# Performance work log

Measured on AMD Instinct MI355X. Metric: run time of the kernel, lower is better.

The kernel has to match this reference:

```python
import jax, jax.numpy as jnp
import numpy as np

GRID = 14  # encoded_image_size

def _grid_edge_index():
    # Exact replica of build_adjacency_matrix().nonzero(): 8-neighbor 14x14 grid.
    edges = []
    for r in range(GRID):
        for c in range(GRID):
            i = r * GRID + c
            for rr in range(max(0, r - 1), min(r + 2, GRID)):
                for cc in range(max(0, c - 1), min(c + 2, GRID)):
                    if rr == r and cc == c:
                        continue
                    edges.append((i, rr * GRID + cc))
    return np.asarray(edges, dtype=np.int64).T  # (2, 1404)


def setup_inputs() -> dict:
    key = jax.random.key(0)
    k1, k2, k3 = jax.random.split(key, 3)
    B, H, W, C, Hid = 128, 14, 14, 2048, 1024
    x = jax.random.normal(k1, (B, H, W, C), dtype=jnp.float32)
    edge_index = jnp.asarray(_grid_edge_index())
    W1 = jax.random.normal(k2, (C, Hid), dtype=jnp.float32) * (1.0 / np.sqrt(C))
    b1 = jnp.zeros((Hid,), jnp.float32)
    W2 = jax.random.normal(k3, (Hid, C), dtype=jnp.float32) * (1.0 / np.sqrt(Hid))
    b2 = jnp.zeros((C,), jnp.float32)
    return {"x": x, "edge_index": edge_index, "W1": W1, "b1": b1, "W2": W2, "b2": b2}


def _gcn_conv(h, W, b, src, dst, dinv):
    # PyG GCNConv: linear transform, symmetric deg-normalized (A+I) aggregation, bias.
    h = h @ W  # [N, out]
    norm = (dinv[src] * dinv[dst])[:, None]
    agg = jax.ops.segment_sum(h[src] * norm, dst, num_segments=h.shape[0])
    agg = agg + h * (dinv * dinv)[:, None]  # self-loop term, norm = 1/deg_i
    return agg + b


def reference(x, edge_index, W1, b1, W2, b2):
    B, H, Wd, C = x.shape
    N = B * H * Wd
    # Faithful to original: permute(0,3,1,2) then reshape(-1, C) (layout-scrambling).
    xf = jnp.transpose(x, (0, 3, 1, 2)).reshape(-1, C)  # [N, C]
    src, dst = edge_index[0], edge_index[1]
    # Degrees over ALL N nodes: self-loop (=1) everywhere + incoming grid edges
    # (only first 196 nodes have grid neighbors; rest are passthrough).
    deg = jnp.ones((N,), xf.dtype).at[dst].add(1.0)
    dinv = jax.lax.rsqrt(deg)
    h = jax.nn.relu(_gcn_conv(xf, W1, b1, src, dst, dinv))
    h = jax.nn.relu(_gcn_conv(h, W2, b2, src, dst, dinv))
    # reshape + permute(0,3,1,2) + permute(0,2,3,1) == identity back to NHWC.
    return h.reshape(B, H, Wd, C)
```

## Files before the change

### kernel.cpp

```cpp
#include <hip/hip_runtime.h>

typedef float  float4_t __attribute__((ext_vector_type(4)));
typedef __bf16 bf16x8   __attribute__((ext_vector_type(8)));

#define BM 128
#define BN 128
#define BK 64

#define GLD16(g, l)                                                        \
    __builtin_amdgcn_global_load_lds(                                      \
        (const __attribute__((address_space(1))) void*)(g),                \
        (__attribute__((address_space(3))) void*)(l), 16, 0, 0)

__global__ void transpose_x_kernel(const float* __restrict__ x, __bf16* __restrict__ A1)
{
    __shared__ float tile[32][33];
    const int b  = blockIdx.z;
    const int pt = blockIdx.y * 32;
    const int ct = blockIdx.x * 32;
    const int tx = threadIdx.x, ty = threadIdx.y;

    const float* xb = x + (size_t)b * 401408;
#pragma unroll
    for (int rr = 0; rr < 4; ++rr) {
        int p = pt + ty + rr * 8;
        if (p < 196) tile[ty + rr * 8][tx] = xb[(size_t)p * 2048 + ct + tx];
    }
    __syncthreads();
    __bf16* ab = A1 + (size_t)b * 401408;
    int p = pt + tx;
    if (p < 196) {
#pragma unroll
        for (int rr = 0; rr < 4; ++rr) {
            int cc = ty + rr * 8;
            ab[(size_t)(ct + cc) * 196 + p] = (__bf16)tile[tx][cc];
        }
    }
}

__global__ void transpose_w_kernel(const float* __restrict__ W, __bf16* __restrict__ Wt,
                                   int K, int N)
{
    __shared__ float tile[32][33];
    const int kt = blockIdx.x * 32, nt = blockIdx.y * 32;
    const int tx = threadIdx.x, ty = threadIdx.y;
#pragma unroll
    for (int rr = 0; rr < 4; ++rr)
        tile[ty + rr * 8][tx] = W[(size_t)(kt + ty + rr * 8) * N + nt + tx];
    __syncthreads();
#pragma unroll
    for (int rr = 0; rr < 4; ++rr)
        Wt[(size_t)(nt + ty + rr * 8) * K + kt + tx] = (__bf16)tile[tx][ty + rr * 8];
}

template<bool OUT_BF16>
__global__ __launch_bounds__(256)
void gemm_bt_kernel(const __bf16* __restrict__ A,
                    const __bf16* __restrict__ Bt,
                    const float* __restrict__ bias,
                    void* __restrict__ out,
                    float* __restrict__ raw_out,
                    int M, int N, int K)
{
    __shared__ __bf16 sA[BM * BK];
    __shared__ __bf16 sB[BN * BK];

    const int tid  = threadIdx.x;
    const int wid  = tid >> 6;
    const int lane = tid & 63;
    const int row0 = blockIdx.y * BM;
    const int col0 = blockIdx.x * BN;
    const int wave_m = (wid >> 1) * 64;
    const int wave_n = (wid & 1) * 64;

    float4_t acc[4][4];
#pragma unroll
    for (int i = 0; i < 4; ++i)
#pragma unroll
        for (int j = 0; j < 4; ++j)
            acc[i][j] = (float4_t){0.f, 0.f, 0.f, 0.f};

    const int lrow = lane >> 3;
    const int lcol = (lane & 7) * 8;
    const int mrow = lane & 15;
    const int kq   = (lane >> 4) * 8;

    for (int k0 = 0; k0 < K; k0 += BK) {
        const __bf16* Ab = A  + (size_t)row0 * K + k0;
        const __bf16* Bb = Bt + (size_t)col0 * K + k0;
#pragma unroll
        for (int t = 0; t < 4; ++t) {
            int chunk = wid * 4 + t;
            int r = chunk * 8 + lrow;
            GLD16(Ab + (size_t)r * K + lcol, sA + chunk * 512);
            GLD16(Bb + (size_t)r * K + lcol, sB + chunk * 512);
        }
        __syncthreads();
#pragma unroll
        for (int kk = 0; kk < BK; kk += 32) {
            bf16x8 af[4], bfr[4];
#pragma unroll
            for (int i = 0; i < 4; ++i)
                af[i] = *(const bf16x8*)&sA[(wave_m + i * 16 + mrow) * BK + kk + kq];
#pragma unroll
            for (int j = 0; j < 4; ++j)
                bfr[j] = *(const bf16x8*)&sB[(wave_n + j * 16 + mrow) * BK + kk + kq];
#pragma unroll
            for (int i = 0; i < 4; ++i)
#pragma unroll
                for (int j = 0; j < 4; ++j)
                    acc[i][j] = __builtin_amdgcn_mfma_f32_16x16x32_bf16(
                        af[i], bfr[j], acc[i][j], 0, 0, 0);
        }
        __syncthreads();
    }

    const int crow = (lane >> 4) * 4;
    const int ccol = lane & 15;
#pragma unroll
    for (int i = 0; i < 4; ++i) {
#pragma unroll
        for (int j = 0; j < 4; ++j) {
            int gcol = col0 + wave_n + j * 16 + ccol;
            float bv = bias[gcol];
#pragma unroll
            for (int r = 0; r < 4; ++r) {
                int grow = row0 + wave_m + i * 16 + crow + r;
                float v = acc[i][j][r];
                if (grow < 196) raw_out[grow * N + gcol] = v;
                float o = fmaxf(v + bv, 0.f);
                if (OUT_BF16) ((__bf16*)out)[(size_t)grow * N + gcol] = (__bf16)o;
                else          ((float*)out)[(size_t)grow * N + gcol] = o;
            }
        }
    }
}

template<typename OutT>
__global__ void fixup_kernel(const float* __restrict__ raw, const float* __restrict__ bias,
                             OutT* __restrict__ out, int N)
{
    const int q = blockIdx.x;
    const int r = q / 14, c = q % 14;
    int nbr[8];
    int cnt = 0;
    for (int rr = (r > 0 ? r - 1 : 0); rr <= (r < 13 ? r + 1 : 13); ++rr)
        for (int cc = (c > 0 ? c - 1 : 0); cc <= (c < 13 ? c + 1 : 13); ++cc)
            if (!(rr == r && cc == c)) nbr[cnt++] = rr * 14 + cc;
    const float dq    = 1.f / sqrtf(1.f + (float)cnt);
    const float wself = 1.f / (1.f + (float)cnt);
    float wn[8];
    for (int t = 0; t < cnt; ++t) {
        int pr = nbr[t] / 14, pc = nbr[t] % 14;
        int pcnt = ((pr < 13 ? pr + 1 : 13) - (pr > 0 ? pr - 1 : 0) + 1) *
                   ((pc < 13 ? pc + 1 : 13) - (pc > 0 ? pc - 1 : 0) + 1) - 1;
        wn[t] = dq / sqrtf(1.f + (float)pcnt);
    }
    for (int ch = threadIdx.x; ch < N; ch += blockDim.x) {
        float s = raw[q * N + ch] * wself;
        for (int t = 0; t < cnt; ++t) s += raw[nbr[t] * N + ch] * wn[t];
        float o = fmaxf(s + bias[ch], 0.f);
        out[(size_t)q * N + ch] = (OutT)o;
    }
}

extern "C" void kernel_launch(void* const* d_in, const int* in_sizes, int n_in,
                              void* d_out, int out_size, void* d_ws, size_t ws_size,
                              hipStream_t stream)
{
    const float* x  = (const float*)d_in[0];
    const float* W1 = (const float*)d_in[2];
    const float* b1 = (const float*)d_in[3];
    const float* W2 = (const float*)d_in[4];
    const float* b2 = (const float*)d_in[5];

    const int M = 25088, C = 2048, Hid = 1024;

    __bf16* A1 = (__bf16*)d_out;

    char* ws = (char*)d_ws;
    __bf16* A2    = (__bf16*)(ws);
    __bf16* W1t   = (__bf16*)(ws + 51380224);
    __bf16* W2t   = (__bf16*)(ws + 55574528);
    float*  h1raw = (float*)(ws + 59768832);
    float*  h2raw = (float*)(ws + 60571648);

    transpose_x_kernel<<<dim3(64, 7, 128), dim3(32, 8), 0, stream>>>(x, A1);
    transpose_w_kernel<<<dim3(C / 32, Hid / 32), dim3(32, 8), 0, stream>>>(W1, W1t, C, Hid);
    transpose_w_kernel<<<dim3(Hid / 32, C / 32), dim3(32, 8), 0, stream>>>(W2, W2t, Hid, C);

    gemm_bt_kernel<true ><<<dim3(Hid / BN, M / BM), 256, 0, stream>>>(
        A1, W1t, b1, (void*)A2, h1raw, M, Hid, C);
    fixup_kernel<__bf16><<<196, 256, 0, stream>>>(h1raw, b1, A2, Hid);

    gemm_bt_kernel<false><<<dim3(C / BN, M / BM), 256, 0, stream>>>(
        A2, W2t, b2, d_out, h2raw, M, C, Hid);
    fixup_kernel<float><<<196, 256, 0, stream>>>(h2raw, b2, (float*)d_out, C);
}
```

Baseline: 760.2 us.

## Remap GEMM block order for XCD-aware L2 reuse and widen transpose/fixup kernels

The GEMM block index is remapped so consecutive block IDs, which are spread round-robin across the 8 XCDs, form groups that share A row tiles and B column tiles within each XCD. The aim is better L2 reuse of A and W tiles. The x transpose now uses 64-channel tiles with 1D threads and writes 8-byte vectors instead of scalar bf16 stores. The fixup kernels are spread over a 2D grid so more blocks run in parallel. Each change adds some index arithmetic, and the transpose writes have alignment constraints because each row is 196 elements.

```diff
diff --git a/kernel.cpp b/kernel.cpp
--- a/kernel.cpp
+++ b/kernel.cpp
@@ -2,6 +2,7 @@
 
 typedef float  float4_t __attribute__((ext_vector_type(4)));
 typedef __bf16 bf16x8   __attribute__((ext_vector_type(8)));
+typedef __bf16 bf16x4   __attribute__((ext_vector_type(4)));
 
 #define BM 128
 #define BN 128
@@ -12,28 +13,39 @@
         (const __attribute__((address_space(1))) void*)(g),                \
         (__attribute__((address_space(3))) void*)(l), 16, 0, 0)
 
-__global__ void transpose_x_kernel(const float* __restrict__ x, __bf16* __restrict__ A1)
-{
-    __shared__ float tile[32][33];
+__global__ __launch_bounds__(256)
+void transpose_x_kernel(const float* __restrict__ x, __bf16* __restrict__ A1)
+{
+    __shared__ float tile[64][33];
     const int b  = blockIdx.z;
     const int pt = blockIdx.y * 32;
-    const int ct = blockIdx.x * 32;
-    const int tx = threadIdx.x, ty = threadIdx.y;
+    const int ct = blockIdx.x * 64;
+    const int t  = threadIdx.x;
 
     const float* xb = x + (size_t)b * 401408;
-#pragma unroll
-    for (int rr = 0; rr < 4; ++rr) {
-        int p = pt + ty + rr * 8;
-        if (p < 196) tile[ty + rr * 8][tx] = xb[(size_t)p * 2048 + ct + tx];
+    const int c  = t & 63;
+    const int pr = t >> 6;
+#pragma unroll
+    for (int pass = 0; pass < 8; ++pass) {
+        int pp = pass * 4 + pr;
+        int p  = pt + pp;
+        if (p < 196) tile[c][pp] = xb[(size_t)p * 2048 + ct + c];
     }
     __syncthreads();
-    __bf16* ab = A1 + (size_t)b * 401408;
-    int p = pt + tx;
-    if (p < 196) {
-#pragma unroll
-        for (int rr = 0; rr < 4; ++rr) {
-            int cc = ty + rr * 8;
-            ab[(size_t)(ct + cc) * 196 + p] = (__bf16)tile[tx][cc];
+
+    const int c2 = t >> 2;
+    const int po = (t & 3) * 8;
+    const int valid = 196 - pt;
+    __bf16* ab = A1 + (size_t)b * 401408 + (size_t)(ct + c2) * 196 + pt + po;
+    if (po < valid) {
+        bf16x4 v0, v1;
+#pragma unroll
+        for (int i = 0; i < 4; ++i) v0[i] = (__bf16)tile[c2][po + i];
+        *(bf16x4*)ab = v0;
+        if (po + 8 <= valid) {
+#pragma unroll
+            for (int i = 0; i < 4; ++i) v1[i] = (__bf16)tile[c2][po + 4 + i];
+            *(bf16x4*)(ab + 4) = v1;
         }
     }
 }
@@ -53,7 +65,7 @@
         Wt[(size_t)(nt + ty + rr * 8) * K + kt + tx] = (__bf16)tile[tx][ty + rr * 8];
 }
 
-template<bool OUT_BF16>
+template<bool OUT_BF16, int NX, int G>
 __global__ __launch_bounds__(256)
 void gemm_bt_kernel(const __bf16* __restrict__ A,
                     const __bf16* __restrict__ Bt,
@@ -68,8 +80,17 @@
     const int tid  = threadIdx.x;
     const int wid  = tid >> 6;
     const int lane = tid & 63;
-    const int row0 = blockIdx.y * BM;
-    const int col0 = blockIdx.x * BN;
+
+    constexpr int NGROUPS = NX / G;
+    constexpr int XPG     = 8 / NGROUPS;
+    const int l   = blockIdx.x + NX * blockIdx.y;
+    const int r8  = l & 7;
+    const int t   = l >> 3;
+    const int gid = r8 % NGROUPS;
+    const int s   = r8 / NGROUPS;
+    const int row0 = ((t / G) * XPG + s) * BM;
+    const int col0 = (gid * G + (t % G)) * BN;
+
     const int wave_m = (wid >> 1) * 64;
     const int wave_n = (wid & 1) * 64;
 
@@ -89,11 +110,11 @@
         const __bf16* Ab = A  + (size_t)row0 * K + k0;
         const __bf16* Bb = Bt + (size_t)col0 * K + k0;
 #pragma unroll
-        for (int t = 0; t < 4; ++t) {
-            int chunk = wid * 4 + t;
-            int r = chunk * 8 + lrow;
-            GLD16(Ab + (size_t)r * K + lcol, sA + chunk * 512);
-            GLD16(Bb + (size_t)r * K + lcol, sB + chunk * 512);
+        for (int tt = 0; tt < 4; ++tt) {
+            int chunk = wid * 4 + tt;
+            int rr = chunk * 8 + lrow;
+            GLD16(Ab + (size_t)rr * K + lcol, sA + chunk * 512);
+            GLD16(Bb + (size_t)rr * K + lcol, sB + chunk * 512);
         }
         __syncthreads();
 #pragma unroll
@@ -117,6 +138,7 @@
 
     const int crow = (lane >> 4) * 4;
     const int ccol = lane & 15;
+    const bool has_raw = row0 < 196;
 #pragma unroll
     for (int i = 0; i < 4; ++i) {
 #pragma unroll
@@ -127,7 +149,7 @@
             for (int r = 0; r < 4; ++r) {
                 int grow = row0 + wave_m + i * 16 + crow + r;
                 float v = acc[i][j][r];
-                if (grow < 196) raw_out[grow * N + gcol] = v;
+                if (has_raw && grow < 196) raw_out[grow * N + gcol] = v;
                 float o = fmaxf(v + bv, 0.f);
                 if (OUT_BF16) ((__bf16*)out)[(size_t)grow * N + gcol] = (__bf16)o;
                 else          ((float*)out)[(size_t)grow * N + gcol] = o;
@@ -156,12 +178,11 @@
                    ((pc < 13 ? pc + 1 : 13) - (pc > 0 ? pc - 1 : 0) + 1) - 1;
         wn[t] = dq / sqrtf(1.f + (float)pcnt);
     }
-    for (int ch = threadIdx.x; ch < N; ch += blockDim.x) {
-        float s = raw[q * N + ch] * wself;
-        for (int t = 0; t < cnt; ++t) s += raw[nbr[t] * N + ch] * wn[t];
-        float o = fmaxf(s + bias[ch], 0.f);
-        out[(size_t)q * N + ch] = (OutT)o;
-    }
+    const int ch = blockIdx.y * 256 + threadIdx.x;
+    float s = raw[q * N + ch] * wself;
+    for (int t = 0; t < cnt; ++t) s += raw[nbr[t] * N + ch] * wn[t];
+    float o = fmaxf(s + bias[ch], 0.f);
+    out[(size_t)q * N + ch] = (OutT)o;
 }
 
 extern "C" void kernel_launch(void* const* d_in, const int* in_sizes, int n_in,
@@ -185,15 +206,15 @@
     float*  h1raw = (float*)(ws + 59768832);
     float*  h2raw = (float*)(ws + 60571648);
 
-    transpose_x_kernel<<<dim3(64, 7, 128), dim3(32, 8), 0, stream>>>(x, A1);
+    transpose_x_kernel<<<dim3(32, 7, 128), 256, 0, stream>>>(x, A1);
     transpose_w_kernel<<<dim3(C / 32, Hid / 32), dim3(32, 8), 0, stream>>>(W1, W1t, C, Hid);
     transpose_w_kernel<<<dim3(Hid / 32, C / 32), dim3(32, 8), 0, stream>>>(W2, W2t, Hid, C);
 
-    gemm_bt_kernel<true ><<<dim3(Hid / BN, M / BM), 256, 0, stream>>>(
+    gemm_bt_kernel<true, 8, 2><<<dim3(Hid / BN, M / BM), 256, 0, stream>>>(
         A1, W1t, b1, (void*)A2, h1raw, M, Hid, C);
-    fixup_kernel<__bf16><<<196, 256, 0, stream>>>(h1raw, b1, A2, Hid);
-
-    gemm_bt_kernel<false><<<dim3(C / BN, M / BM), 256, 0, stream>>>(
+    fixup_kernel<__bf16><<<dim3(196, Hid / 256), 256, 0, stream>>>(h1raw, b1, A2, Hid);
+
+    gemm_bt_kernel<false, 16, 4><<<dim3(C / BN, M / BM), 256, 0, stream>>>(
         A2, W2t, b2, d_out, h2raw, M, C, Hid);
-    fixup_kernel<float><<<196, 256, 0, stream>>>(h2raw, b2, (float*)d_out, C);
-}
+    fixup_kernel<float><<<dim3(196, C / 256), 256, 0, stream>>>(h2raw, b2, (float*)d_out, C);
+}
```

Measured after the change: 749.1 us. No clear change (-1.5%).
